# Kernel optimization log

Measured on AMD Instinct MI355X. Metric: run time of the kernel, lower is better.

The kernel has to match this reference:

```python
import jax, jax.numpy as jnp
import numpy as np

# ShapeNet category -> contiguous segment range (16 categories, 50 segments)
SEG_LENS = np.array([4, 2, 2, 4, 4, 3, 3, 2, 4, 2, 6, 2, 3, 3, 3, 3], dtype=np.int32)
SHIFTS = np.concatenate([[0], np.cumsum(SEG_LENS)[:-1]]).astype(np.int32)
NUM_CAT = 16
IN_F = 256
MAX_SEG_COUNT = 6   # max len(seg) over categories
MAX_SEG = 49        # max segment id
N_PTS = 32768
BN_EPS = 1e-5


def setup_inputs() -> dict:
    key = jax.random.key(0)
    k1, k2, k3, k4 = jax.random.split(key, 4)
    features = jax.random.normal(k1, (N_PTS, IN_F), dtype=jnp.float32)
    W1 = jax.random.normal(k2, (IN_F, NUM_CAT * IN_F), dtype=jnp.float32) * (1.0 / np.sqrt(IN_F))
    gamma = jnp.ones((NUM_CAT * IN_F,), dtype=jnp.float32)
    beta = jnp.zeros((NUM_CAT * IN_F,), dtype=jnp.float32)
    Wc = jax.random.normal(k3, (NUM_CAT, IN_F, MAX_SEG_COUNT), dtype=jnp.float32) * (1.0 / np.sqrt(IN_F))
    bias = jnp.zeros((MAX_SEG_COUNT,), dtype=jnp.float32)
    cats = jax.random.randint(k4, (N_PTS,), 0, NUM_CAT, dtype=jnp.int32)
    return {
        "features": features, "W1": W1, "gamma": gamma, "beta": beta,
        "Wc": Wc, "bias": bias, "cats": cats,
        "shifts": jnp.asarray(SHIFTS), "seg_lens": jnp.asarray(SEG_LENS),
    }


def reference(features, W1, gamma, beta, Wc, bias, cats, shifts, seg_lens):
    N, F = features.shape
    C, _, S = Wc.shape
    # channel_rasing: Linear(bias=False) -> BatchNorm1d (batch stats) -> LeakyReLU(0.2)
    x = features @ W1                              # [N, C*F]
    mu = x.mean(axis=0)
    var = x.var(axis=0)                            # biased, as BatchNorm
    x = (x - mu) * jax.lax.rsqrt(var + BN_EPS) * gamma + beta
    x = jnp.where(x >= 0, x, 0.2 * x)              # LeakyReLU(0.2); Dropout = identity (eval)
    # UnaryConv: per-category matmul + shared bias -> [C, N, S]
    x = x.reshape(N, C, F)
    feats = jnp.einsum('ncf,cfs->cns', x, Wc) + bias
    # gather the assigned category's logits per point -> [N, S]
    logits = feats[cats, jnp.arange(N)]
    lsm = jax.nn.log_softmax(logits, axis=-1)
    # scatter (expressed as gather) into per-category segment ranges -> [N, MAX_SEG+1]
    sh = shifts[cats]                              # [N]
    ln = seg_lens[cats]                            # [N]
    k = jnp.arange(MAX_SEG + 1, dtype=jnp.int32)   # [50]
    j = k[None, :] - sh[:, None]                   # [N, 50]
    valid = (j >= 0) & (j < ln[:, None])
    jc = jnp.clip(j, 0, S - 1)
    out = jnp.where(valid, jnp.take_along_axis(lsm, jc, axis=1), 0.0)
    return out
```

## Files before the change

kernel.cpp:

```cpp
#include <hip/hip_runtime.h>
#include <hip/hip_bf16.h>
#include <math.h>

#define N_PTS 32768
#define IN_F  256
#define NUM_CAT 16
#define CF    4096
#define NSEG  6
#define OUTK  50
#define BN_EPS 1e-5f

typedef unsigned short u16;
typedef __attribute__((ext_vector_type(8))) short bf16x8;
typedef __attribute__((ext_vector_type(4))) float f32x4;
typedef __attribute__((ext_vector_type(8))) unsigned short u16x8;

#define OFF_G     0u
#define OFF_FBAR  65536u
#define OFF_SCALE 65792u
#define OFF_SHIFT 69888u
#define OFF_INT   73984u
#define OFF_FB    107424u
#define OFF_FBT   4301728u
#define OFF_W1T   8496032u
#define OFF_GP    9020320u
#define OFF_VP    OFF_GP
#define OFF_MU    (OFF_GP + 32768u)
#define IO_CATOFF 16
#define IO_ORDER  67
#define IO_PC     32835

__device__ __forceinline__ void gload_lds16(const void* g, void* l) {
    __builtin_amdgcn_global_load_lds(
        (const __attribute__((address_space(1))) void*)g,
        (__attribute__((address_space(3))) void*)l,
        16, 0, 0);
}
__device__ __forceinline__ u16 f2bf(float f) {
    unsigned int u = __float_as_uint(f);
    return (u16)((u + 0x7FFF + ((u >> 16) & 1)) >> 16);
}
__device__ __forceinline__ float bf2f(u16 h) {
    return __uint_as_float((unsigned int)h << 16);
}

__global__ __launch_bounds__(256) void kA(const float* __restrict__ F,
                                          const float* __restrict__ W1,
                                          const int* __restrict__ cats,
                                          u16* __restrict__ Fb,
                                          u16* __restrict__ FbT,
                                          u16* __restrict__ W1T,
                                          float* __restrict__ ws) {
    const int b = blockIdx.x;
    const int tid = threadIdx.x;
    __shared__ u16 T[64][72];
    __shared__ int h[16];

    if (b < 2048) {
        const int pb = b >> 2, fb = b & 3;
        const int p0 = pb * 64, f0 = fb * 64;
        {
            int p = tid >> 2, fq = tid & 3;
            const float* src = &F[(size_t)(p0 + p) * IN_F + f0 + fq * 16];
            u16x8 o0, o1;
            float4 v0 = *(const float4*)&src[0];
            float4 v1 = *(const float4*)&src[4];
            float4 v2 = *(const float4*)&src[8];
            float4 v3 = *(const float4*)&src[12];
            o0[0]=f2bf(v0.x); o0[1]=f2bf(v0.y); o0[2]=f2bf(v0.z); o0[3]=f2bf(v0.w);
            o0[4]=f2bf(v1.x); o0[5]=f2bf(v1.y); o0[6]=f2bf(v1.z); o0[7]=f2bf(v1.w);
            o1[0]=f2bf(v2.x); o1[1]=f2bf(v2.y); o1[2]=f2bf(v2.z); o1[3]=f2bf(v2.w);
            o1[4]=f2bf(v3.x); o1[5]=f2bf(v3.y); o1[6]=f2bf(v3.z); o1[7]=f2bf(v3.w);
            u16* dst = &Fb[(size_t)(p0 + p) * IN_F + f0 + fq * 16];
            *(u16x8*)dst = o0; *(u16x8*)&dst[8] = o1;
            *(u16x8*)&T[p][fq * 16] = o0; *(u16x8*)&T[p][fq * 16 + 8] = o1;
        }
        __syncthreads();
        {
            int f = tid >> 2, pq = tid & 3;
            u16x8 a0, a1;
#pragma unroll
            for (int m = 0; m < 8; m++) { a0[m] = T[pq*16 + m][f]; a1[m] = T[pq*16 + 8 + m][f]; }
            u16* dst = &FbT[(size_t)(f0 + f) * N_PTS + p0 + pq * 16];
            *(u16x8*)dst = a0; *(u16x8*)&dst[8] = a1;
        }
    } else if (b < 2304) {
        const int bb = b - 2048;
        const int kb = bb & 3, jb = bb >> 2;
        {
            int kk = tid >> 2, j4 = (tid & 3) * 16;
            const float* src = &W1[(size_t)(kb * 64 + kk) * CF + jb * 64 + j4];
#pragma unroll
            for (int q = 0; q < 4; q++) {
                float4 v = *(const float4*)&src[q * 4];
                T[kk][j4 + q * 4 + 0] = f2bf(v.x); T[kk][j4 + q * 4 + 1] = f2bf(v.y);
                T[kk][j4 + q * 4 + 2] = f2bf(v.z); T[kk][j4 + q * 4 + 3] = f2bf(v.w);
            }
        }
        __syncthreads();
        {
            int jj = tid >> 2, ks = (tid & 3) * 16;
            int c = jb >> 2, n = (jb & 3) * 64 + jj;
            u16* dst = &W1T[((size_t)(c * 256 + n)) * 256 + kb * 64 + ks];
            u16x8 o0, o1;
#pragma unroll
            for (int m = 0; m < 8; m++) { o0[m] = T[ks + m][jj]; o1[m] = T[ks + 8 + m][jj]; }
            *(u16x8*)dst = o0;
            *(u16x8*)&dst[8] = o1;
        }
    } else {
        const int hb = b - 2304;
        if (tid < 16) h[tid] = 0;
        __syncthreads();
        const int n0 = hb * 512;
        atomicAdd(&h[cats[n0 + tid]], 1);
        atomicAdd(&h[cats[n0 + 256 + tid]], 1);
        __syncthreads();
        if (tid < 16) {
            u16* pc = (u16*)((int*)(ws + OFF_INT) + IO_PC);
            pc[hb * 16 + tid] = (u16)h[tid];
        }
    }
}

__global__ __launch_bounds__(512) void kB(const u16* __restrict__ FbT,
                                          float* __restrict__ ws,
                                          int nchunk, int Kc) {
    const int tid = threadIdx.x;
    __shared__ __align__(16) u16 SA[2][8192];
    __shared__ __align__(16) u16 SB[2][8192];
    __shared__ float ps[8];

    if ((int)blockIdx.x < 3 * nchunk) {
        const int tile = blockIdx.x % 3, chunk = blockIdx.x / 3;
        const int i0 = (tile == 2) ? 128 : 0;
        const int j0 = (tile == 0) ? 0 : 128;
        const bool diag = (tile != 1);
        const int r0 = chunk * Kc;
        const int wv = tid >> 6, ln = tid & 63, g = ln >> 4, r16 = ln & 15;

        const int f0_ = (wv * 2 + 0) * 64 + ln, f1_ = (wv * 2 + 1) * 64 + ln;
        const int row0 = f0_ >> 3, u0 = f0_ & 7, k0off = ((u0 ^ (row0 & 7)) << 3);
        const int row1 = f1_ >> 3, u1 = f1_ & 7, k1off = ((u1 ^ (row1 & 7)) << 3);

        f32x4 acc8[8];
#pragma unroll
        for (int nt = 0; nt < 8; nt++)
#pragma unroll
            for (int i = 0; i < 4; i++) acc8[nt][i] = 0.f;

        const int nslab = Kc >> 6;
#define KB_STAGE(s, bf)                                                            \
        {   int p0s = r0 + (s) * 64;                                               \
            gload_lds16(FbT + (size_t)(i0 + row0) * N_PTS + p0s + k0off,           \
                        (char*)SA[bf] + (wv * 2 + 0) * 1024);                      \
            gload_lds16(FbT + (size_t)(i0 + row1) * N_PTS + p0s + k1off,           \
                        (char*)SA[bf] + (wv * 2 + 1) * 1024);                      \
            if (!diag) {                                                           \
                gload_lds16(FbT + (size_t)(j0 + row0) * N_PTS + p0s + k0off,       \
                            (char*)SB[bf] + (wv * 2 + 0) * 1024);                  \
                gload_lds16(FbT + (size_t)(j0 + row1) * N_PTS + p0s + k1off,       \
                            (char*)SB[bf] + (wv * 2 + 1) * 1024);                  \
            }                                                                      \
        }

        KB_STAGE(0, 0);
        __syncthreads();
        for (int s = 0; s < nslab; s++) {
            const int bf = s & 1;
            if (s + 1 < nslab) KB_STAGE(s + 1, bf ^ 1);
            const char* BB = diag ? (const char*)SA[bf] : (const char*)SB[bf];
#pragma unroll
            for (int ks = 0; ks < 2; ks++) {
                const int row = wv * 16 + r16;
                const int pha = ((ks * 4 + g) ^ (row & 7)) * 16;
                bf16x8 a = *(const bf16x8*)((const char*)SA[bf] + row * 128 + pha);
#pragma unroll
                for (int nt = 0; nt < 8; nt++) {
                    const int cr = nt * 16 + r16;
                    const int phb = ((ks * 4 + g) ^ (cr & 7)) * 16;
                    bf16x8 bb = *(const bf16x8*)(BB + cr * 128 + phb);
                    acc8[nt] = __builtin_amdgcn_mfma_f32_16x16x32_bf16(a, bb, acc8[nt], 0, 0, 0);
                }
            }
            __syncthreads();
        }
        float* Gp = ws + OFF_GP + (size_t)chunk * 49152 + tile * 16384;
#pragma unroll
        for (int nt = 0; nt < 8; nt++)
#pragma unroll
            for (int i = 0; i < 4; i++)
                Gp[(wv * 16 + g * 4 + i) * 128 + nt * 16 + r16] = acc8[nt][i];
    } else {
        const int row = blockIdx.x - 3 * nchunk;
        const u16* r = FbT + (size_t)row * N_PTS;
        float s = 0.f;
        for (int i = tid * 8; i < N_PTS; i += 4096) {
            u16x8 v = *(const u16x8*)&r[i];
#pragma unroll
            for (int m = 0; m < 8; m++) s += bf2f(v[m]);
        }
#pragma unroll
        for (int off = 32; off >= 1; off >>= 1) s += __shfl_xor(s, off);
        if ((tid & 63) == 0) ps[tid >> 6] = s;
        __syncthreads();
        if (tid == 0) {
            float t = 0.f;
#pragma unroll
            for (int w = 0; w < 8; w++) t += ps[w];
            ws[OFF_FBAR + row] = t * (1.0f / N_PTS);
        }
    }
}

__global__ __launch_bounds__(256) void kC(const int* __restrict__ cats,
                                          float* __restrict__ ws, int nchunk) {
    const int tid = threadIdx.x;
    int* wi = (int*)(ws + OFF_INT);
    __shared__ int tot[16], bbs[16], coff[17], lh[16];

    if (blockIdx.x < 192) {
        const int e = blockIdx.x * 256 + tid;
        const float* p = ws + OFF_GP + e;
        float s = 0.f;
        for (int c = 0; c < nchunk; c++) s += p[(size_t)c * 49152];
        const int t = e >> 14, x = (e >> 7) & 127, y = e & 127;
        const int a = ((t == 2) ? 128 : 0) + x;
        const int bcol = ((t == 0) ? 0 : 128) + y;
        ws[OFF_G + a * 256 + bcol] = s;
        ws[OFF_G + bcol * 256 + a] = s;
    } else {
        const int sb = blockIdx.x - 192;
        const u16* pc = (const u16*)(wi + IO_PC);
        if (tid < 16) {
            int T = 0, B = 0;
            for (int b2 = 0; b2 < 64; b2++) {
                int v = pc[b2 * 16 + tid];
                T += v;
                if (b2 < sb) B += v;
            }
            tot[tid] = T; bbs[tid] = B; lh[tid] = 0;
        }
        __syncthreads();
        if (tid == 0) {
            int co = 0;
            for (int c = 0; c < 16; c++) { coff[c] = co; co += tot[c]; }
            coff[16] = co;
        }
        __syncthreads();
        const int n0 = sb * 512;
        {
            int cA = cats[n0 + tid];
            int rA = atomicAdd(&lh[cA], 1);
            wi[IO_ORDER + coff[cA] + bbs[cA] + rA] = n0 + tid;
        }
        {
            int cB = cats[n0 + 256 + tid];
            int rB = atomicAdd(&lh[cB], 1);
            wi[IO_ORDER + coff[cB] + bbs[cB] + rB] = n0 + 256 + tid;
        }
        if (sb == 0 && tid < 17) wi[IO_CATOFF + tid] = coff[tid];
    }
}

__global__ __launch_bounds__(256) void k2b_stats(const float* __restrict__ W1,
                                                 const u16* __restrict__ W1T,
                                                 float* __restrict__ ws) {
    const int tid = threadIdx.x;
    const int jg = blockIdx.x >> 3, sp = blockIdx.x & 7;
    const int j0 = jg * 32;
    const int c = jg >> 3, n0 = (jg & 7) * 32;
    __shared__ float pwv[32][4], pwm[32][4];

    float acc[32];
#pragma unroll
    for (int jj = 0; jj < 32; jj++) acc[jj] = 0.f;

    const float* Gs = ws + OFF_G + (size_t)(sp * 32) * 256;
#pragma unroll 2
    for (int b = 0; b < 32; b++) {
        const float g = Gs[b * 256 + tid];
        const float* wrow = W1 + (size_t)(sp * 32 + b) * CF + j0;
#pragma unroll
        for (int jj = 0; jj < 32; jj++)
            acc[jj] += g * wrow[jj];
    }

    const int lane = tid & 63, wave = tid >> 6;
    const float fb = ws[OFF_FBAR + tid];
#pragma unroll
    for (int jj = 0; jj < 32; jj++) {
        const float wk = bf2f(W1T[((size_t)(c * 256 + n0 + jj)) * 256 + tid]);
        float v = wk * acc[jj];
#pragma unroll
        for (int off = 32; off >= 1; off >>= 1) v += __shfl_xor(v, off);
        if (lane == 0) pwv[jj][wave] = v;
        if (sp == 0) {
            float m = fb * wk;
#pragma unroll
            for (int off = 32; off >= 1; off >>= 1) m += __shfl_xor(m, off);
            if (lane == 0) pwm[jj][wave] = m;
        }
    }
    __syncthreads();
    if (tid < 32) {
        float v = pwv[tid][0] + pwv[tid][1] + pwv[tid][2] + pwv[tid][3];
        ws[OFF_VP + sp * 4096 + j0 + tid] = v;
        if (sp == 0) {
            float m = pwm[tid][0] + pwm[tid][1] + pwm[tid][2] + pwm[tid][3];
            ws[OFF_MU + j0 + tid] = m;
        }
    }
}

__global__ __launch_bounds__(256) void k2c_finish(const float* __restrict__ gamma,
                                                  const float* __restrict__ beta,
                                                  float* __restrict__ ws) {
    const int j = blockIdx.x * 256 + threadIdx.x;
    float v = 0.f;
#pragma unroll
    for (int sp = 0; sp < 8; sp++) v += ws[OFF_VP + sp * 4096 + j];
    const float mu = ws[OFF_MU + j];
    const float var = v * (1.0f / N_PTS) - mu * mu;
    const float sc = gamma[j] * rsqrtf(var + BN_EPS);
    ws[OFF_SCALE + j] = sc;
    ws[OFF_SHIFT + j] = beta[j] - mu * sc;
}

__global__ __launch_bounds__(512, 4) void k5_mfma(const u16* __restrict__ Fb,
                                                  const u16* __restrict__ W1T,
                                                  const float* __restrict__ Wc,
                                                  const float* __restrict__ bias,
                                                  const int* __restrict__ shifts,
                                                  const int* __restrict__ seg_lens,
                                                  const float* __restrict__ ws,
                                                  float* __restrict__ out) {
    const int* wi = (const int*)(ws + OFF_INT);
    const int t = blockIdx.x;
    int c = -1, base = 0, npts = 0;
    {
        int ts = 0;
#pragma unroll
        for (int cc = 0; cc < 16; cc++) {
            int o0 = wi[IO_CATOFF + cc], o1 = wi[IO_CATOFF + cc + 1];
            int cn = o1 - o0, ntl = (cn + 63) >> 6;
            if (c < 0 && t < ts + ntl) {
                int lt = t - ts;
                c = cc; base = o0 + lt * 64; npts = min(64, cn - lt * 64);
            }
            ts += ntl;
        }
    }
    if (c < 0) return;
    const int tid = threadIdx.x;
    const int wv = tid >> 6, ln = tid & 63;
    const int g = ln >> 4, r16 = ln & 15, r7 = r16 & 7;

    __shared__ __align__(16) u16 Fl[16384];
    __shared__ float red[64][8][8];
    __shared__ int plds[64];

    if (tid < 64) plds[tid] = wi[IO_ORDER + base + min(tid, npts - 1)];
    const int col0 = wv * 32 + r16, col1 = col0 + 16;
    const float sc0 = ws[OFF_SCALE + c * 256 + col0];
    const float sc1 = ws[OFF_SCALE + c * 256 + col1];
    const float sh0 = ws[OFF_SHIFT + c * 256 + col0];
    const float sh1 = ws[OFF_SHIFT + c * 256 + col1];
    const float biasj = ((tid & 7) < 6) ? bias[tid & 7] : 0.f;
    const int shc = shifts[c], lnc = seg_lens[c];
    __syncthreads();

#pragma unroll
    for (int s = 0; s < 4; s++) {
        int flat = (wv * 4 + s) * 64 + ln;
        int pt = flat >> 5, u = flat & 31;
        const u16* src = Fb + (size_t)plds[pt] * 256 + ((u ^ (pt & 7)) << 3);
        gload_lds16(src, (char*)Fl + (size_t)(wv * 4 + s) * 1024);
    }

    const u16* W1Tc = W1T + (size_t)c * 65536;
    const u16* wp0 = W1Tc + (size_t)col0 * 256 + g * 8;
    const u16* wp1 = W1Tc + (size_t)col1 * 256 + g * 8;

    __syncthreads();

    f32x4 acc[4][2];
#pragma unroll
    for (int mt = 0; mt < 4; mt++)
#pragma unroll
        for (int nt = 0; nt < 2; nt++)
#pragma unroll
            for (int i = 0; i < 4; i++) acc[mt][nt][i] = 0.f;

    bf16x8 bf0[2], bf1[2];
    bf0[0] = *(const bf16x8*)(wp0);
    bf1[0] = *(const bf16x8*)(wp1);

#pragma unroll
    for (int kc = 0; kc < 8; kc++) {
        if (kc < 7) {
            bf0[(kc + 1) & 1] = *(const bf16x8*)(wp0 + (kc + 1) * 32);
            bf1[(kc + 1) & 1] = *(const bf16x8*)(wp1 + (kc + 1) * 32);
        }
#pragma unroll
        for (int mt = 0; mt < 4; mt++) {
            int row = mt * 16 + r16;
            int ph = ((kc * 4 + g) ^ r7) * 16;
            bf16x8 af = *(const bf16x8*)((const char*)Fl + (size_t)row * 512 + ph);
            acc[mt][0] = __builtin_amdgcn_mfma_f32_16x16x32_bf16(af, bf0[kc & 1], acc[mt][0], 0, 0, 0);
            acc[mt][1] = __builtin_amdgcn_mfma_f32_16x16x32_bf16(af, bf1[kc & 1], acc[mt][1], 0, 0, 0);
        }
    }
    __builtin_amdgcn_sched_barrier(0);

    float wc0[6], wc1[6];
#pragma unroll
    for (int s = 0; s < 6; s++) {
        wc0[s] = Wc[(size_t)c * 1536 + col0 * 6 + s];
        wc1[s] = Wc[(size_t)c * 1536 + col1 * 6 + s];
    }
#pragma unroll
    for (int mt = 0; mt < 4; mt++)
#pragma unroll
        for (int i = 0; i < 4; i++) {
            float x0 = acc[mt][0][i] * sc0 + sh0;  x0 = (x0 >= 0.f) ? x0 : 0.2f * x0;
            float x1 = acc[mt][1][i] * sc1 + sh1;  x1 = (x1 >= 0.f) ? x1 : 0.2f * x1;
            float pl[6];
#pragma unroll
            for (int s = 0; s < 6; s++) pl[s] = x0 * wc0[s] + x1 * wc1[s];
#pragma unroll
            for (int s = 0; s < 6; s++) {
                pl[s] += __shfl_xor(pl[s], 1);
                pl[s] += __shfl_xor(pl[s], 2);
                pl[s] += __shfl_xor(pl[s], 4);
                pl[s] += __shfl_xor(pl[s], 8);
            }
            if (r16 == 0) {
                int row = mt * 16 + g * 4 + i;
#pragma unroll
                for (int s = 0; s < 6; s++) red[row][wv][s] = pl[s];
            }
        }
    __syncthreads();

    {
        const int lpt = tid >> 3, j = tid & 7;
        float v = -1e30f;
        if (j < 6) {
            v = biasj;
#pragma unroll
            for (int w = 0; w < 8; w++) v += red[lpt][w][j];
        }
        float mx = v;
        mx = fmaxf(mx, __shfl_xor(mx, 1));
        mx = fmaxf(mx, __shfl_xor(mx, 2));
        mx = fmaxf(mx, __shfl_xor(mx, 4));
        float e = (j < 6) ? expf(v - mx) : 0.f;
        float se = e;
        se += __shfl_xor(se, 1);
        se += __shfl_xor(se, 2);
        se += __shfl_xor(se, 4);
        float lsm = v - (mx + logf(se));
        if (lpt < npts) {
            const int pid = plds[lpt];
            float* orow = out + (size_t)pid * OUTK;
            const int gb = ln & 56;
#pragma unroll
            for (int it = 0; it < 7; it++) {
                int k = j + it * 8;
                int jj = k - shc;
                int jc = min(max(jj, 0), 5);
                float val = __shfl(lsm, gb | jc);
                if (k < OUTK)
                    orow[k] = (jj >= 0 && jj < lnc) ? val : 0.f;
            }
        }
    }
}

extern "C" void kernel_launch(void* const* d_in, const int* in_sizes, int n_in,
                              void* d_out, int out_size, void* d_ws, size_t ws_size,
                              hipStream_t stream) {
    const float* F      = (const float*)d_in[0];
    const float* W1     = (const float*)d_in[1];
    const float* gamma  = (const float*)d_in[2];
    const float* beta   = (const float*)d_in[3];
    const float* Wc     = (const float*)d_in[4];
    const float* bias   = (const float*)d_in[5];
    const int*  cats    = (const int*)d_in[6];
    const int*  shifts  = (const int*)d_in[7];
    const int*  seglens = (const int*)d_in[8];
    float* out = (float*)d_out;
    float* ws  = (float*)d_ws;
    u16* Fb  = (u16*)(ws + OFF_FB);
    u16* FbT = (u16*)(ws + OFF_FBT);
    u16* W1T = (u16*)(ws + OFF_W1T);

    int nchunk = 64;
    if (ws_size < ((size_t)OFF_GP + 49152ull * 64) * 4) nchunk = 32;
    const int Kc = N_PTS / nchunk;

    hipLaunchKernelGGL(kA,         dim3(2368), dim3(256), 0, stream,
                       F, W1, cats, Fb, FbT, W1T, ws);
    hipLaunchKernelGGL(kB,         dim3(3 * nchunk + 256), dim3(512), 0, stream,
                       FbT, ws, nchunk, Kc);
    hipLaunchKernelGGL(kC,         dim3(256),  dim3(256), 0, stream, cats, ws, nchunk);
    hipLaunchKernelGGL(k2b_stats,  dim3(1024), dim3(256), 0, stream, W1, W1T, ws);
    hipLaunchKernelGGL(k2c_finish, dim3(16),   dim3(256), 0, stream, gamma, beta, ws);
    hipLaunchKernelGGL(k5_mfma,    dim3(528),  dim3(512), 0, stream,
                       Fb, W1T, Wc, bias, shifts, seglens, ws, out);
}
```

Before: 124.3 us.

## Use MFMA for the per-category Wc projection and preload all W1 fragments

The fp32 projection onto the 6 segment logits used per-lane FMAs plus a 4-step shuffle reduction. It is replaced by writing the BN+LeakyReLU activations back to LDS as bf16 and running one extra MFMA per row tile against a bf16 packed Wc fragment. All eight k-chunks of W1 are now issued up front through inline-asm global loads instead of double-buffered loads, and block IDs are remapped to interleave tiles across categories. The activations and Wc are rounded to bf16, which costs precision, and the 16 fragments held at once add register pressure.

```diff
diff --git a/kernel.cpp b/kernel.cpp
--- a/kernel.cpp
+++ b/kernel.cpp
@@ -13,6 +13,7 @@
 typedef unsigned short u16;
 typedef __attribute__((ext_vector_type(8))) short bf16x8;
 typedef __attribute__((ext_vector_type(4))) float f32x4;
+typedef __attribute__((ext_vector_type(4))) unsigned int u32x4;
 typedef __attribute__((ext_vector_type(8))) unsigned short u16x8;
 
 #define OFF_G     0u
@@ -336,7 +337,8 @@
                                                   const float* __restrict__ ws,
                                                   float* __restrict__ out) {
     const int* wi = (const int*)(ws + OFF_INT);
-    const int t = blockIdx.x;
+    const int bid = blockIdx.x;
+    const int t = (bid & 7) * 66 + (bid >> 3);
     int c = -1, base = 0, npts = 0;
     {
         int ts = 0;
@@ -368,6 +370,13 @@
     const float sh1 = ws[OFF_SHIFT + c * 256 + col1];
     const float biasj = ((tid & 7) < 6) ? bias[tid & 7] : 0.f;
     const int shc = shifts[c], lnc = seg_lens[c];
+
+    bf16x8 bwc;
+#pragma unroll
+    for (int j = 0; j < 8; j++) {
+        float v = (r16 < 6) ? Wc[(size_t)c * 1536 + (wv * 32 + g * 8 + j) * 6 + r16] : 0.f;
+        bwc[j] = (short)f2bf(v);
+    }
     __syncthreads();
 
 #pragma unroll
@@ -379,8 +388,16 @@
     }
 
     const u16* W1Tc = W1T + (size_t)c * 65536;
-    const u16* wp0 = W1Tc + (size_t)col0 * 256 + g * 8;
-    const u16* wp1 = W1Tc + (size_t)col1 * 256 + g * 8;
+    unsigned long long a0 = (unsigned long long)(W1Tc + (size_t)col0 * 256 + g * 8);
+    unsigned long long a1 = (unsigned long long)(W1Tc + (size_t)col1 * 256 + g * 8);
+    u32x4 wr[16];
+#pragma unroll
+    for (int kc = 0; kc < 8; kc++) {
+        asm volatile("global_load_dwordx4 %0, %1, off offset:%2"
+                     : "=v"(wr[kc * 2])     : "v"(a0), "i"(kc * 64));
+        asm volatile("global_load_dwordx4 %0, %1, off offset:%2"
+                     : "=v"(wr[kc * 2 + 1]) : "v"(a1), "i"(kc * 64));
+    }
 
     __syncthreads();
 
@@ -392,55 +409,53 @@
 #pragma unroll
             for (int i = 0; i < 4; i++) acc[mt][nt][i] = 0.f;
 
-    bf16x8 bf0[2], bf1[2];
-    bf0[0] = *(const bf16x8*)(wp0);
-    bf1[0] = *(const bf16x8*)(wp1);
-
 #pragma unroll
     for (int kc = 0; kc < 8; kc++) {
-        if (kc < 7) {
-            bf0[(kc + 1) & 1] = *(const bf16x8*)(wp0 + (kc + 1) * 32);
-            bf1[(kc + 1) & 1] = *(const bf16x8*)(wp1 + (kc + 1) * 32);
-        }
+        bf16x8 b0 = __builtin_bit_cast(bf16x8, wr[kc * 2]);
+        bf16x8 b1 = __builtin_bit_cast(bf16x8, wr[kc * 2 + 1]);
 #pragma unroll
         for (int mt = 0; mt < 4; mt++) {
             int row = mt * 16 + r16;
             int ph = ((kc * 4 + g) ^ r7) * 16;
             bf16x8 af = *(const bf16x8*)((const char*)Fl + (size_t)row * 512 + ph);
-            acc[mt][0] = __builtin_amdgcn_mfma_f32_16x16x32_bf16(af, bf0[kc & 1], acc[mt][0], 0, 0, 0);
-            acc[mt][1] = __builtin_amdgcn_mfma_f32_16x16x32_bf16(af, bf1[kc & 1], acc[mt][1], 0, 0, 0);
-        }
-    }
-    __builtin_amdgcn_sched_barrier(0);
-
-    float wc0[6], wc1[6];
-#pragma unroll
-    for (int s = 0; s < 6; s++) {
-        wc0[s] = Wc[(size_t)c * 1536 + col0 * 6 + s];
-        wc1[s] = Wc[(size_t)c * 1536 + col1 * 6 + s];
-    }
+            acc[mt][0] = __builtin_amdgcn_mfma_f32_16x16x32_bf16(af, b0, acc[mt][0], 0, 0, 0);
+            acc[mt][1] = __builtin_amdgcn_mfma_f32_16x16x32_bf16(af, b1, acc[mt][1], 0, 0, 0);
+        }
+    }
+
+    __syncthreads();
+
 #pragma unroll
     for (int mt = 0; mt < 4; mt++)
 #pragma unroll
         for (int i = 0; i < 4; i++) {
+            const int row = mt * 16 + g * 4 + i;
             float x0 = acc[mt][0][i] * sc0 + sh0;  x0 = (x0 >= 0.f) ? x0 : 0.2f * x0;
             float x1 = acc[mt][1][i] * sc1 + sh1;  x1 = (x1 >= 0.f) ? x1 : 0.2f * x1;
-            float pl[6];
-#pragma unroll
-            for (int s = 0; s < 6; s++) pl[s] = x0 * wc0[s] + x1 * wc1[s];
-#pragma unroll
-            for (int s = 0; s < 6; s++) {
-                pl[s] += __shfl_xor(pl[s], 1);
-                pl[s] += __shfl_xor(pl[s], 2);
-                pl[s] += __shfl_xor(pl[s], 4);
-                pl[s] += __shfl_xor(pl[s], 8);
-            }
-            if (r16 == 0) {
-                int row = mt * 16 + g * 4 + i;
-#pragma unroll
-                for (int s = 0; s < 6; s++) red[row][wv][s] = pl[s];
-            }
-        }
+            {
+                const int u = (col0 >> 3) ^ (row & 7);
+                *(u16*)((char*)Fl + row * 512 + u * 16 + (col0 & 7) * 2) = f2bf(x0);
+            }
+            {
+                const int u = (col1 >> 3) ^ (row & 7);
+                *(u16*)((char*)Fl + row * 512 + u * 16 + (col1 & 7) * 2) = f2bf(x1);
+            }
+        }
+    __syncthreads();
+
+    f32x4 zero = {0.f, 0.f, 0.f, 0.f};
+#pragma unroll
+    for (int mt = 0; mt < 4; mt++) {
+        const int ar = mt * 16 + r16;
+        const int au = (wv * 4 + g) ^ (ar & 7);
+        bf16x8 ax = *(const bf16x8*)((const char*)Fl + ar * 512 + au * 16);
+        f32x4 pc = __builtin_amdgcn_mfma_f32_16x16x32_bf16(ax, bwc, zero, 0, 0, 0);
+        if (r16 < 8) {
+#pragma unroll
+            for (int i = 0; i < 4; i++)
+                red[mt * 16 + g * 4 + i][wv][r16] = pc[i];
+        }
+    }
     __syncthreads();
 
     {
```

Result: faster. 108.0 us (-13.2%).
